# Kernel tuning notes

Hardware: AMD Instinct MI355X
Metric: run time of the kernel (lower is better)

## Reference

```python
import jax, jax.numpy as jnp
import numpy as np

B, L1, CTX_TXT, C, NH, HD = 2, 4096, 512, 2048, 16, 128
IMG_LEN = 257           # hard-coded image-context length in WanI2VCrossAttentionProcessor
L2 = IMG_LEN + CTX_TXT
EPS = 1e-6


def setup_inputs() -> dict:
    key = jax.random.key(0)
    ks = jax.random.split(key, 16)
    s = 0.02
    w = lambda k: jax.random.normal(k, (C, C), jnp.float32) * s
    bvec = lambda k: jax.random.normal(k, (C,), jnp.float32) * s
    return {
        "x": jax.random.normal(ks[0], (B, L1, C), jnp.float32),
        "context": jax.random.normal(ks[1], (B, L2, C), jnp.float32),
        "context_lens": jax.random.randint(ks[2], (B,), 1, CTX_TXT + 1, jnp.int32),
        "Wq": w(ks[3]), "bq": bvec(ks[4]), "gq": jnp.ones((C,), jnp.float32),
        "Wk": w(ks[5]), "bk": bvec(ks[6]), "gk": jnp.ones((C,), jnp.float32),
        "Wv": w(ks[7]), "bv": bvec(ks[8]),
        "Wki": w(ks[9]), "bki": bvec(ks[10]), "gki": jnp.ones((C,), jnp.float32),
        "Wvi": w(ks[11]), "bvi": bvec(ks[12]),
        "Wo": w(ks[13]), "bo": bvec(ks[14]),
    }


def rms_norm(x, g):
    # RMSNorm over full channel dim (applied before head reshape, as in source)
    return x * jax.lax.rsqrt(jnp.mean(x * x, axis=-1, keepdims=True) + EPS) * g


def attention(q, k, v, key_mask=None):
    # q: [b, Lq, n, d]; k, v: [b, Lk, n, d]
    scale = 1.0 / np.sqrt(HD).astype(np.float32)
    scores = jnp.einsum('bqnd,bknd->bnqk', q, k) * scale
    if key_mask is not None:
        scores = jnp.where(key_mask, scores, jnp.finfo(scores.dtype).min)
    probs = jax.nn.softmax(scores, axis=-1)
    return jnp.einsum('bnqk,bknd->bqnd', probs, v)


def reference(x, context, context_lens, Wq, bq, gq, Wk, bk, gk, Wv, bv,
              Wki, bki, gki, Wvi, bvi, Wo, bo):
    b = x.shape[0]
    ctx_img = context[:, :IMG_LEN]
    ctx_txt = context[:, IMG_LEN:]

    q = rms_norm(x @ Wq + bq, gq).reshape(b, -1, NH, HD)
    k = rms_norm(ctx_txt @ Wk + bk, gk).reshape(b, -1, NH, HD)
    v = (ctx_txt @ Wv + bv).reshape(b, -1, NH, HD)
    k_img = rms_norm(ctx_img @ Wki + bki, gki).reshape(b, -1, NH, HD)
    v_img = (ctx_img @ Wvi + bvi).reshape(b, -1, NH, HD)

    img_x = attention(q, k_img, v_img)  # no k_lens on image branch
    key_mask = (jnp.arange(CTX_TXT)[None, :] < context_lens[:, None])[:, None, None, :]
    txt_x = attention(q, k, v, key_mask)

    out = (txt_x + img_x).reshape(b, -1, NH * HD)
    return out @ Wo + bo
```

## Files before the change

kernel.cpp:

```cpp
#include <hip/hip_runtime.h>

typedef unsigned short u16;
typedef short short8 __attribute__((ext_vector_type(8)));
typedef float f32x4 __attribute__((ext_vector_type(4)));
typedef unsigned short u16x4 __attribute__((ext_vector_type(4)));

__device__ __forceinline__ u16 f2bf(float f) {
  unsigned u = __builtin_bit_cast(unsigned, f);
  u += 0x7fffu + ((u >> 16) & 1u);
  return (u16)(u >> 16);
}
__device__ __forceinline__ float bf2f(u16 s) {
  unsigned u = ((unsigned)s) << 16;
  return __builtin_bit_cast(float, u);
}
__device__ __forceinline__ unsigned cvtpk_bf16(float a, float b) {
  unsigned r;
  asm("v_cvt_pk_bf16_f32 %0, %1, %2" : "=v"(r) : "v"(a), "v"(b));
  return r;
}

#if __has_builtin(__builtin_amdgcn_exp2f)
#define EXP2F(x) __builtin_amdgcn_exp2f(x)
#else
#define EXP2F(x) exp2f(x)
#endif

#define MFMA32(a, b, c) __builtin_amdgcn_mfma_f32_16x16x32_bf16(a, b, c, 0, 0, 0)

#define GLDS16(gp, lp)                                                         \
  __builtin_amdgcn_global_load_lds(                                            \
      (__attribute__((address_space(1))) void*)(gp),                           \
      (__attribute__((address_space(3))) void*)(lp), 16, 0, 0)

__global__ __launch_bounds__(256) void cast_bf16_k(const float* __restrict__ in,
                                                   u16* __restrict__ out, int n4) {
  int i = blockIdx.x * 256 + threadIdx.x;
  if (i >= n4) return;
  float4 v = ((const float4*)in)[i];
  u16x4 o = { f2bf(v.x), f2bf(v.y), f2bf(v.z), f2bf(v.w) };
  ((u16x4*)out)[i] = o;
}

__global__ __launch_bounds__(256) void transw_k(const float* W0, const float* W1,
                                                const float* W2, const float* W3,
                                                const float* W4, const float* W5,
                                                u16* __restrict__ Wt) {
  int z = blockIdx.z;
  const float* W = z == 0 ? W0 : z == 1 ? W1 : z == 2 ? W2 : z == 3 ? W3 : z == 4 ? W4 : W5;
  u16* T = Wt + (size_t)z * 2048 * 2048;
  __shared__ float tile[64][65];
  int k0 = blockIdx.x * 64, n0 = blockIdx.y * 64;
  int c4 = (threadIdx.x & 15) * 4;
  int r = threadIdx.x >> 4;
#pragma unroll
  for (int i = 0; i < 4; ++i) {
    int row = r + i * 16;
    float4 v = *(const float4*)(W + (size_t)(k0 + row) * 2048 + n0 + c4);
    tile[row][c4 + 0] = v.x; tile[row][c4 + 1] = v.y;
    tile[row][c4 + 2] = v.z; tile[row][c4 + 3] = v.w;
  }
  __syncthreads();
#pragma unroll
  for (int i = 0; i < 4; ++i) {
    int nrow = r + i * 16;
    u16x4 o = { f2bf(tile[c4 + 0][nrow]), f2bf(tile[c4 + 1][nrow]),
                f2bf(tile[c4 + 2][nrow]), f2bf(tile[c4 + 3][nrow]) };
    *(u16x4*)(T + (size_t)(n0 + nrow) * 2048 + k0 + c4) = o;
  }
}

struct GemmJob {
  const u16* A; const u16* Bt; const float* bias; void* out;
  int M; int mode; int ldo;
};
struct GemmJobs { GemmJob j[8]; };

__global__ __launch_bounds__(256) void gemm_k(GemmJobs jobs) {
  GemmJob J = jobs.j[blockIdx.z];
  const int m0 = blockIdx.x * 128;
  if (m0 >= J.M) return;
  const int n0 = blockIdx.y * 128;
  __shared__ u16 Asm[128 * 32];
  __shared__ u16 Bsm[128 * 32];
  const int tid = threadIdx.x;
  const int lane = tid & 63;
  const int l15 = lane & 15, quad = lane >> 4;
  const int wave = tid >> 6;
  const int wr = (wave >> 1) * 64, wc = (wave & 1) * 64;
  f32x4 acc[4][4] = {};
  const int g0 = tid, g1 = tid + 256;
  const u16* ag0 = J.A + (size_t)(m0 + (g0 >> 2)) * 2048 + (g0 & 3) * 8;
  const u16* ag1 = J.A + (size_t)(m0 + (g1 >> 2)) * 2048 + (g1 & 3) * 8;
  const u16* bg0 = J.Bt + (size_t)(n0 + (g0 >> 2)) * 2048 + (g0 & 3) * 8;
  const u16* bg1 = J.Bt + (size_t)(n0 + (g1 >> 2)) * 2048 + (g1 & 3) * 8;
  u16* al0 = Asm + g0 * 8; u16* al1 = Asm + g1 * 8;
  u16* bl0 = Bsm + g0 * 8; u16* bl1 = Bsm + g1 * 8;
  for (int k0 = 0; k0 < 2048; k0 += 32) {
    GLDS16(ag0 + k0, al0);
    GLDS16(ag1 + k0, al1);
    GLDS16(bg0 + k0, bl0);
    GLDS16(bg1 + k0, bl1);
    __syncthreads();
    short8 af[4], bf[4];
#pragma unroll
    for (int mi = 0; mi < 4; ++mi)
      af[mi] = *(const short8*)(Asm + (wr + mi * 16 + l15) * 32 + quad * 8);
#pragma unroll
    for (int ni = 0; ni < 4; ++ni)
      bf[ni] = *(const short8*)(Bsm + (wc + ni * 16 + l15) * 32 + quad * 8);
#pragma unroll
    for (int mi = 0; mi < 4; ++mi)
#pragma unroll
      for (int ni = 0; ni < 4; ++ni)
        acc[mi][ni] = __builtin_amdgcn_mfma_f32_16x16x32_bf16(af[mi], bf[ni], acc[mi][ni], 0, 0, 0);
    __syncthreads();
  }
#pragma unroll
  for (int mi = 0; mi < 4; ++mi) {
#pragma unroll
    for (int ni = 0; ni < 4; ++ni) {
      int nn = n0 + wc + ni * 16 + l15;
      float bv = J.bias[nn];
#pragma unroll
      for (int r = 0; r < 4; ++r) {
        int mm = m0 + wr + mi * 16 + quad * 4 + r;
        if (mm >= J.M) continue;
        float v = acc[mi][ni][r] + bv;
        if (J.mode == 0) {
          ((u16*)J.out)[(size_t)mm * J.ldo + nn] = f2bf(v);
        } else if (J.mode == 1) {
          int ml = mm & 31;
          int mp = (mm & ~31) | (((ml >> 2) & 3) * 8 + (ml >> 4) * 4 + (ml & 3));
          ((u16*)J.out)[(size_t)nn * J.ldo + mp] = f2bf(v);
        } else {
          ((float*)J.out)[(size_t)mm * J.ldo + nn] = v;
        }
      }
    }
  }
}

__global__ __launch_bounds__(512, 2) void gemm256_k(const u16* __restrict__ A,
                                                    const u16* __restrict__ Bt,
                                                    const float* __restrict__ bias,
                                                    void* __restrict__ out,
                                                    int mode) {
  const int m0 = blockIdx.x * 256, n0 = blockIdx.y * 256;
  __shared__ u16 lds[2][2][256 * 32];
  const int tid = threadIdx.x, lane = tid & 63;
  const int l15 = lane & 15, quad = lane >> 4;
  const int wave = tid >> 6;
  const int wr = wave >> 2;
  const int wc = wave & 3;
  const int srow = tid >> 2;
  const int sc = ((tid & 3) ^ ((srow >> 1) & 3)) * 8;
  const u16* Ag = A + (size_t)(m0 + srow) * 2048 + sc;
  const u16* Bg = Bt + (size_t)(n0 + srow) * 2048 + sc;
  const int lxor = (l15 >> 1) & 3;
  f32x4 acc[8][4] = {};

  auto stage = [&](int buf, int kt) {
    const size_t ko = (size_t)kt * 32;
    u16* dA = &lds[buf][0][tid * 8];
    u16* dB = &lds[buf][1][tid * 8];
    GLDS16(Ag + ko, dA);
    GLDS16(Ag + (size_t)128 * 2048 + ko, dA + 4096);
    GLDS16(Bg + ko, dB);
    GLDS16(Bg + (size_t)128 * 2048 + ko, dB + 4096);
  };

  stage(0, 0);
  for (int t = 0; t < 64; ++t) {
    const int cb = t & 1;
    __syncthreads();
    if (t + 1 < 64) stage(cb ^ 1, t + 1);
    const u16* Ab = &lds[cb][0][(size_t)wr * 128 * 32];
    const u16* Bb = &lds[cb][1][0];
    short8 bfr[4];
#pragma unroll
    for (int ni = 0; ni < 4; ++ni) {
      const int rn = wc * 64 + ni * 16 + l15;
      bfr[ni] = *(const short8*)(Bb + rn * 32 + ((quad ^ lxor) * 8));
    }
#pragma unroll
    for (int mi = 0; mi < 8; ++mi) {
      const int rm = mi * 16 + l15;
      short8 a = *(const short8*)(Ab + rm * 32 + ((quad ^ lxor) * 8));
      __builtin_amdgcn_s_setprio(1);
#pragma unroll
      for (int ni = 0; ni < 4; ++ni)
        acc[mi][ni] = MFMA32(a, bfr[ni], acc[mi][ni]);
      __builtin_amdgcn_s_setprio(0);
    }
  }
#pragma unroll
  for (int mi = 0; mi < 8; ++mi) {
#pragma unroll
    for (int ni = 0; ni < 4; ++ni) {
      const int nn = n0 + wc * 64 + ni * 16 + l15;
      const float bv = bias[nn];
      const int mm = m0 + wr * 128 + mi * 16 + quad * 4;
      if (mode == 0) {
        u16* op = (u16*)out + (size_t)mm * 2048 + nn;
#pragma unroll
        for (int r = 0; r < 4; ++r) op[(size_t)r * 2048] = f2bf(acc[mi][ni][r] + bv);
      } else {
        float* op = (float*)out + (size_t)mm * 2048 + nn;
#pragma unroll
        for (int r = 0; r < 4; ++r) op[(size_t)r * 2048] = acc[mi][ni][r] + bv;
      }
    }
  }
}

__global__ __launch_bounds__(256) void rmsnorm_k(u16* __restrict__ buf,
                                                 const float* __restrict__ g) {
  const int row = blockIdx.x, tid = threadIdx.x;
  u16* p = buf + (size_t)row * 2048 + tid * 8;
  short8 v = *(short8*)p;
  float x[8]; float s = 0.f;
#pragma unroll
  for (int i = 0; i < 8; ++i) { x[i] = bf2f((u16)v[i]); s += x[i] * x[i]; }
#pragma unroll
  for (int o = 1; o < 64; o <<= 1) s += __shfl_xor(s, o, 64);
  __shared__ float ws4[4];
  if ((tid & 63) == 0) ws4[tid >> 6] = s;
  __syncthreads();
  float tot = ws4[0] + ws4[1] + ws4[2] + ws4[3];
  float scale = rsqrtf(tot * (1.0f / 2048.0f) + 1e-6f);
  const float* gp = g + tid * 8;
  short8 o8;
#pragma unroll
  for (int i = 0; i < 8; ++i) o8[i] = (short)f2bf(x[i] * scale * gp[i]);
  *(short8*)p = o8;
}

__global__ __launch_bounds__(256) void attn_k(const u16* __restrict__ Q,
                                              const u16* __restrict__ Kt,
                                              const u16* __restrict__ Vt,
                                              const u16* __restrict__ Ki,
                                              const u16* __restrict__ Vi,
                                              const int* __restrict__ lens,
                                              u16* __restrict__ out) {
  const int b = blockIdx.z, h = blockIdx.y;
  const int tid = threadIdx.x, lane = tid & 63, wave = tid >> 6;
  const int l15 = lane & 15, quad = lane >> 4;
  const int qbase = blockIdx.x * 128 + wave * 32;
  const float scale2 = 0.12752358514837517f;
  const float NEGINF = -__builtin_inff();
  __shared__ u16 Ksm[2][32 * 128];
  __shared__ u16 Vsm[2][128 * 32];

  short8 qf[2][4];
#pragma unroll
  for (int h2 = 0; h2 < 2; ++h2) {
    const u16* qb = Q + ((size_t)(b * 4096 + qbase + h2 * 16 + l15)) * 2048 + h * 128 + quad * 8;
#pragma unroll
    for (int kc = 0; kc < 4; ++kc) qf[h2][kc] = *(const short8*)(qb + kc * 32);
  }

  const int krow = tid >> 4;
  const int kcc = ((tid & 15) ^ (krow & 7)) * 8;
  const int vd = tid >> 2;
  const int vcs = ((tid & 3) ^ ((tid >> 3) & 3)) * 8;
  const int kxor = l15 & 7;
  const int vxor = (l15 >> 1) & 3;

  f32x4 accv[2][8];
  u16x4 oimg[2][8];
  float run_m[2], run_l[2];

  auto phase = [&](const u16* Kb, const u16* Vb, int Lv, int ldv) {
    run_m[0] = run_m[1] = NEGINF;
    run_l[0] = run_l[1] = 0.f;
#pragma unroll
    for (int h2 = 0; h2 < 2; ++h2)
#pragma unroll
      for (int dt = 0; dt < 8; ++dt)
#pragma unroll
        for (int r = 0; r < 4; ++r) accv[h2][dt][r] = 0.f;
    const u16* kg0 = Kb + (size_t)krow * 2048 + kcc;
    const u16* kg1 = kg0 + 16 * 2048;
    const u16* vg0 = Vb + (size_t)vd * ldv + vcs;
    const u16* vg1 = vg0 + (size_t)64 * ldv;
    const int ntiles = (Lv + 31) >> 5;
    GLDS16(kg0, &Ksm[0][tid * 8]);
    GLDS16(kg1, &Ksm[0][2048 + tid * 8]);
    GLDS16(vg0, &Vsm[0][tid * 8]);
    GLDS16(vg1, &Vsm[0][2048 + tid * 8]);
    __syncthreads();
    for (int t = 0; t < ntiles; ++t) {
      const u16* Ks = Ksm[t & 1];
      const u16* Vs = Vsm[t & 1];
      if (t + 1 < ntiles) {
        const int kvn = (t + 1) * 32;
        u16* kd = Ksm[(t + 1) & 1];
        u16* vdp = Vsm[(t + 1) & 1];
        GLDS16(kg0 + (size_t)kvn * 2048, kd + tid * 8);
        GLDS16(kg1 + (size_t)kvn * 2048, kd + 2048 + tid * 8);
        GLDS16(vg0 + kvn, vdp + tid * 8);
        GLDS16(vg1 + kvn, vdp + 2048 + tid * 8);
      }

      short8 kf0[4], kf1[4];
#pragma unroll
      for (int kc = 0; kc < 4; ++kc) {
        int c0 = ((kc * 4 + quad) ^ kxor) * 8;
        kf0[kc] = *(const short8*)(Ks + l15 * 128 + c0);
        kf1[kc] = *(const short8*)(Ks + (16 + l15) * 128 + c0);
      }
      f32x4 s0[2], s1[2];
#pragma unroll
      for (int h2 = 0; h2 < 2; ++h2)
#pragma unroll
        for (int r = 0; r < 4; ++r) { s0[h2][r] = 0.f; s1[h2][r] = 0.f; }
      __builtin_amdgcn_s_setprio(1);
#pragma unroll
      for (int h2 = 0; h2 < 2; ++h2)
#pragma unroll
        for (int kc = 0; kc < 4; ++kc) {
          s0[h2] = MFMA32(kf0[kc], qf[h2][kc], s0[h2]);
          s1[h2] = MFMA32(kf1[kc], qf[h2][kc], s1[h2]);
        }
      __builtin_amdgcn_s_setprio(0);
      const int kv0 = t * 32;
      if (kv0 + 32 > Lv) {
#pragma unroll
        for (int h2 = 0; h2 < 2; ++h2)
#pragma unroll
          for (int r = 0; r < 4; ++r) {
            const int k0i = kv0 + quad * 4 + r;
            if (k0i >= Lv) s0[h2][r] = NEGINF;
            if (k0i + 16 >= Lv) s1[h2][r] = NEGINF;
          }
      }
      float al[2];
      short8 pf[2];
#pragma unroll
      for (int h2 = 0; h2 < 2; ++h2) {
        float mx = fmaxf(fmaxf(fmaxf(s0[h2][0], s0[h2][1]), fmaxf(s0[h2][2], s0[h2][3])),
                         fmaxf(fmaxf(s1[h2][0], s1[h2][1]), fmaxf(s1[h2][2], s1[h2][3])));
        mx = fmaxf(mx, __shfl_xor(mx, 16, 64));
        mx = fmaxf(mx, __shfl_xor(mx, 32, 64));
        const float nm = fmaxf(run_m[h2], mx);
        al[h2] = EXP2F((run_m[h2] - nm) * scale2);
        run_m[h2] = nm;
        const float nmc = -nm * scale2;
        float p0[4], p1[4], psum = 0.f;
#pragma unroll
        for (int r = 0; r < 4; ++r) {
          p0[r] = EXP2F(__builtin_fmaf(s0[h2][r], scale2, nmc));
          p1[r] = EXP2F(__builtin_fmaf(s1[h2][r], scale2, nmc));
          psum += p0[r] + p1[r];
        }
        run_l[h2] = __builtin_fmaf(run_l[h2], al[h2], psum);
        union { short8 s8; unsigned u[4]; } pp;
        pp.u[0] = cvtpk_bf16(p0[0], p0[1]);
        pp.u[1] = cvtpk_bf16(p0[2], p0[3]);
        pp.u[2] = cvtpk_bf16(p1[0], p1[1]);
        pp.u[3] = cvtpk_bf16(p1[2], p1[3]);
        pf[h2] = pp.s8;
      }
      if (t != 0 && __ballot((al[0] < 1.0f) || (al[1] < 1.0f))) {
#pragma unroll
        for (int h2 = 0; h2 < 2; ++h2)
#pragma unroll
          for (int dt = 0; dt < 8; ++dt)
#pragma unroll
            for (int r = 0; r < 4; ++r) accv[h2][dt][r] *= al[h2];
      }
      __builtin_amdgcn_s_setprio(1);
#pragma unroll
      for (int dt = 0; dt < 8; ++dt) {
        short8 vf = *(const short8*)(Vs + (dt * 16 + l15) * 32 + ((quad ^ vxor) * 8));
        accv[0][dt] = MFMA32(vf, pf[0], accv[0][dt]);
        accv[1][dt] = MFMA32(vf, pf[1], accv[1][dt]);
      }
      __builtin_amdgcn_s_setprio(0);
      __syncthreads();
    }
  };

  const u16* Kb_i = Ki + (size_t)(b * 288) * 2048 + h * 128;
  const u16* Vb_i = Vi + ((size_t)(b * 16 + h) * 128) * 288;
  phase(Kb_i, Vb_i, 257, 288);
#pragma unroll
  for (int h2 = 0; h2 < 2; ++h2) {
    float a = run_l[h2] + __shfl_xor(run_l[h2], 16, 64);
    float lt = a + __shfl_xor(a, 32, 64);
    float inv = 1.0f / lt;
#pragma unroll
    for (int dt = 0; dt < 8; ++dt) {
      u16x4 w = { f2bf(accv[h2][dt][0] * inv), f2bf(accv[h2][dt][1] * inv),
                  f2bf(accv[h2][dt][2] * inv), f2bf(accv[h2][dt][3] * inv) };
      oimg[h2][dt] = w;
    }
  }
  const u16* Kb_t = Kt + (size_t)(b * 512) * 2048 + h * 128;
  const u16* Vb_t = Vt + ((size_t)(b * 16 + h) * 128) * 512;
  phase(Kb_t, Vb_t, lens[b], 512);
#pragma unroll
  for (int h2 = 0; h2 < 2; ++h2) {
    float a = run_l[h2] + __shfl_xor(run_l[h2], 16, 64);
    float lt = a + __shfl_xor(a, 32, 64);
    float inv = 1.0f / lt;
    u16* ob = out + ((size_t)(b * 4096 + qbase + h2 * 16 + l15)) * 2048 + h * 128 + quad * 4;
#pragma unroll
    for (int dt = 0; dt < 8; ++dt) {
      u16x4 w = { f2bf(bf2f(oimg[h2][dt][0]) + accv[h2][dt][0] * inv),
                  f2bf(bf2f(oimg[h2][dt][1]) + accv[h2][dt][1] * inv),
                  f2bf(bf2f(oimg[h2][dt][2]) + accv[h2][dt][2] * inv),
                  f2bf(bf2f(oimg[h2][dt][3]) + accv[h2][dt][3] * inv) };
      *(u16x4*)(ob + dt * 16) = w;
    }
  }
}

extern "C" void kernel_launch(void* const* d_in, const int* in_sizes, int n_in,
                              void* d_out, int out_size, void* d_ws, size_t ws_size,
                              hipStream_t stream) {
  const float* x   = (const float*)d_in[0];
  const float* ctx = (const float*)d_in[1];
  const int* lens  = (const int*)d_in[2];
  const float* Wq  = (const float*)d_in[3];
  const float* bq  = (const float*)d_in[4];
  const float* gq  = (const float*)d_in[5];
  const float* Wk  = (const float*)d_in[6];
  const float* bk  = (const float*)d_in[7];
  const float* gk  = (const float*)d_in[8];
  const float* Wv  = (const float*)d_in[9];
  const float* bv  = (const float*)d_in[10];
  const float* Wki = (const float*)d_in[11];
  const float* bki = (const float*)d_in[12];
  const float* gki = (const float*)d_in[13];
  const float* Wvi = (const float*)d_in[14];
  const float* bvi = (const float*)d_in[15];
  const float* Wo  = (const float*)d_in[16];
  const float* bo  = (const float*)d_in[17];
  float* out = (float*)d_out;

  char* p = (char*)d_ws;
  u16* x_bf   = (u16*)p; p += (size_t)8192 * 2048 * 2;
  u16* ctx_bf = (u16*)p; p += (size_t)2 * 769 * 2048 * 2;
  u16* Wt     = (u16*)p; p += (size_t)6 * 2048 * 2048 * 2;
  u16* Qb     = (u16*)p; p += (size_t)8192 * 2048 * 2;
  u16* Ktxt   = (u16*)p; p += (size_t)2 * 512 * 2048 * 2;
  u16* Vtt    = (u16*)p; p += (size_t)2 * 16 * 128 * 512 * 2;
  u16* Kimg   = (u16*)p; p += (size_t)2 * 288 * 2048 * 2;
  u16* Vti    = (u16*)p; p += (size_t)2 * 16 * 128 * 288 * 2;
  u16* attn_o = x_bf;

  cast_bf16_k<<<16384, 256, 0, stream>>>(x, x_bf, 8192 * 2048 / 4);
  cast_bf16_k<<<3076, 256, 0, stream>>>(ctx, ctx_bf, 2 * 769 * 2048 / 4);
  transw_k<<<dim3(32, 32, 6), 256, 0, stream>>>(Wq, Wk, Wv, Wki, Wvi, Wo, Wt);

  gemm256_k<<<dim3(32, 8), 512, 0, stream>>>(x_bf, Wt + 0ull * 4194304, bq, Qb, 0);

  GemmJobs jc = {};
  for (int b = 0; b < 2; ++b) {
    const u16* txtA = ctx_bf + (size_t)(b * 769 + 257) * 2048;
    const u16* imgA = ctx_bf + (size_t)(b * 769) * 2048;
    jc.j[0 + b] = { txtA, Wt + 1ull * 4194304, bk,  Ktxt + (size_t)b * 512 * 2048, 512, 0, 2048 };
    jc.j[2 + b] = { txtA, Wt + 2ull * 4194304, bv,  Vtt  + (size_t)b * 2048 * 512, 512, 1, 512 };
    jc.j[4 + b] = { imgA, Wt + 3ull * 4194304, bki, Kimg + (size_t)b * 288 * 2048, 257, 0, 2048 };
    jc.j[6 + b] = { imgA, Wt + 4ull * 4194304, bvi, Vti  + (size_t)b * 2048 * 288, 257, 1, 288 };
  }
  gemm_k<<<dim3(4, 16, 8), 256, 0, stream>>>(jc);

  rmsnorm_k<<<8192, 256, 0, stream>>>(Qb, gq);
  rmsnorm_k<<<1024, 256, 0, stream>>>(Ktxt, gk);
  rmsnorm_k<<<576, 256, 0, stream>>>(Kimg, gki);

  attn_k<<<dim3(32, 16, 2), 256, 0, stream>>>(Qb, Ktxt, Vtt, Kimg, Vti, lens, attn_o);

  gemm256_k<<<dim3(32, 8), 512, 0, stream>>>(attn_o, Wt + 5ull * 4194304, bo, out, 1);
}
```

Baseline: 589.2 us.

## Triple-buffer attention K/V tiles and swizzle block order for XCD locality

The attention kernel's K/V shared-memory pipeline moves from double to triple buffering. Loads are issued two tiles ahead, and a vmcnt wait plus one barrier per iteration replaces the trailing __syncthreads, so global-to-LDS latency overlaps more compute. The block index is also remapped so that consecutive blocks, which are spread round-robin over the 8 XCDs, share the same (batch, head) on each XCD, aiming for better L2 reuse of K/V. The cost is 50% more LDS per block, which may lower occupancy, plus redundant dummy loads near the tail.

```diff
diff --git a/kernel.cpp b/kernel.cpp
--- a/kernel.cpp
+++ b/kernel.cpp
@@ -243,14 +243,18 @@
                                               const u16* __restrict__ Vi,
                                               const int* __restrict__ lens,
                                               u16* __restrict__ out) {
-  const int b = blockIdx.z, h = blockIdx.y;
+  const int lid = blockIdx.x + 32 * (blockIdx.y + 16 * blockIdx.z);
+  const int w = (lid & 7) * 128 + (lid >> 3);
+  const int qx = w & 31, hb = w >> 5;
+  const int h = hb & 15, b = hb >> 4;
+
   const int tid = threadIdx.x, lane = tid & 63, wave = tid >> 6;
   const int l15 = lane & 15, quad = lane >> 4;
-  const int qbase = blockIdx.x * 128 + wave * 32;
+  const int qbase = qx * 128 + wave * 32;
   const float scale2 = 0.12752358514837517f;
   const float NEGINF = -__builtin_inff();
-  __shared__ u16 Ksm[2][32 * 128];
-  __shared__ u16 Vsm[2][128 * 32];
+  __shared__ u16 Ksm[3][32 * 128];
+  __shared__ u16 Vsm[3][128 * 32];
 
   short8 qf[2][4];
 #pragma unroll
@@ -285,23 +289,31 @@
     const u16* vg0 = Vb + (size_t)vd * ldv + vcs;
     const u16* vg1 = vg0 + (size_t)64 * ldv;
     const int ntiles = (Lv + 31) >> 5;
-    GLDS16(kg0, &Ksm[0][tid * 8]);
-    GLDS16(kg1, &Ksm[0][2048 + tid * 8]);
-    GLDS16(vg0, &Vsm[0][tid * 8]);
-    GLDS16(vg1, &Vsm[0][2048 + tid * 8]);
-    __syncthreads();
+    __builtin_amdgcn_s_barrier();
+    {
+      GLDS16(kg0, &Ksm[0][tid * 8]);
+      GLDS16(kg1, &Ksm[0][2048 + tid * 8]);
+      GLDS16(vg0, &Vsm[0][tid * 8]);
+      GLDS16(vg1, &Vsm[0][2048 + tid * 8]);
+      const size_t k1 = (ntiles > 1) ? 32 : 0;
+      GLDS16(kg0 + k1 * 2048, &Ksm[1][tid * 8]);
+      GLDS16(kg1 + k1 * 2048, &Ksm[1][2048 + tid * 8]);
+      GLDS16(vg0 + k1, &Vsm[1][tid * 8]);
+      GLDS16(vg1 + k1, &Vsm[1][2048 + tid * 8]);
+    }
+    int cb = 0, nb = 2;
     for (int t = 0; t < ntiles; ++t) {
-      const u16* Ks = Ksm[t & 1];
-      const u16* Vs = Vsm[t & 1];
-      if (t + 1 < ntiles) {
-        const int kvn = (t + 1) * 32;
-        u16* kd = Ksm[(t + 1) & 1];
-        u16* vdp = Vsm[(t + 1) & 1];
-        GLDS16(kg0 + (size_t)kvn * 2048, kd + tid * 8);
-        GLDS16(kg1 + (size_t)kvn * 2048, kd + 2048 + tid * 8);
-        GLDS16(vg0 + kvn, vdp + tid * 8);
-        GLDS16(vg1 + kvn, vdp + 2048 + tid * 8);
-      }
+      asm volatile("s_waitcnt vmcnt(4)" ::: "memory");
+      __builtin_amdgcn_s_barrier();
+      {
+        const size_t kn = (size_t)((t + 2 < ntiles) ? (t + 2) * 32 : 0);
+        GLDS16(kg0 + kn * 2048, &Ksm[nb][tid * 8]);
+        GLDS16(kg1 + kn * 2048, &Ksm[nb][2048 + tid * 8]);
+        GLDS16(vg0 + kn, &Vsm[nb][tid * 8]);
+        GLDS16(vg1 + kn, &Vsm[nb][2048 + tid * 8]);
+      }
+      const u16* Ks = Ksm[cb];
+      const u16* Vs = Vsm[cb];
 
       short8 kf0[4], kf1[4];
 #pragma unroll
@@ -378,7 +390,8 @@
         accv[1][dt] = MFMA32(vf, pf[1], accv[1][dt]);
       }
       __builtin_amdgcn_s_setprio(0);
-      __syncthreads();
+      cb = (cb == 2) ? 0 : cb + 1;
+      nb = (nb == 2) ? 0 : nb + 1;
     }
   };
 
@@ -392,9 +405,9 @@
     float inv = 1.0f / lt;
 #pragma unroll
     for (int dt = 0; dt < 8; ++dt) {
-      u16x4 w = { f2bf(accv[h2][dt][0] * inv), f2bf(accv[h2][dt][1] * inv),
-                  f2bf(accv[h2][dt][2] * inv), f2bf(accv[h2][dt][3] * inv) };
-      oimg[h2][dt] = w;
+      u16x4 w2 = { f2bf(accv[h2][dt][0] * inv), f2bf(accv[h2][dt][1] * inv),
+                   f2bf(accv[h2][dt][2] * inv), f2bf(accv[h2][dt][3] * inv) };
+      oimg[h2][dt] = w2;
     }
   }
   const u16* Kb_t = Kt + (size_t)(b * 512) * 2048 + h * 128;
@@ -408,11 +421,11 @@
     u16* ob = out + ((size_t)(b * 4096 + qbase + h2 * 16 + l15)) * 2048 + h * 128 + quad * 4;
 #pragma unroll
     for (int dt = 0; dt < 8; ++dt) {
-      u16x4 w = { f2bf(bf2f(oimg[h2][dt][0]) + accv[h2][dt][0] * inv),
-                  f2bf(bf2f(oimg[h2][dt][1]) + accv[h2][dt][1] * inv),
-                  f2bf(bf2f(oimg[h2][dt][2]) + accv[h2][dt][2] * inv),
-                  f2bf(bf2f(oimg[h2][dt][3]) + accv[h2][dt][3] * inv) };
-      *(u16x4*)(ob + dt * 16) = w;
+      u16x4 w2 = { f2bf(bf2f(oimg[h2][dt][0]) + accv[h2][dt][0] * inv),
+                   f2bf(bf2f(oimg[h2][dt][1]) + accv[h2][dt][1] * inv),
+                   f2bf(bf2f(oimg[h2][dt][2]) + accv[h2][dt][2] * inv),
+                   f2bf(bf2f(oimg[h2][dt][3]) + accv[h2][dt][3] * inv) };
+      *(u16x4*)(ob + dt * 16) = w2;
     }
   }
 }
```

Measured after the change: 595.1 us. Within noise of the previous version (+1.0%).
